# Kernel optimization log

Measured on AMD Instinct MI355X. Metric: run time of the kernel, lower is better.

## Reference

```python
import jax, jax.numpy as jnp
import numpy as np


def setup_inputs() -> dict:
    key = jax.random.key(0)
    ks = jax.random.split(key, 8)
    B, Te, De, Dd, H = 64, 1024, 1024, 1024, 1024
    return {
        "encoder_outputs": jax.random.normal(ks[0], (B, Te, De), jnp.float32),
        "decoder_outputs": jax.random.normal(ks[1], (B, 1, Dd), jnp.float32),
        "Wa_w": jax.random.normal(ks[2], (H, Dd), jnp.float32) * 0.02,
        "Wa_b": jax.random.normal(ks[3], (H,), jnp.float32) * 0.02,
        "Ua_w": jax.random.normal(ks[4], (H, De), jnp.float32) * 0.02,
        "Ua_b": jax.random.normal(ks[5], (H,), jnp.float32) * 0.02,
        "Va_w": jax.random.normal(ks[6], (1, H), jnp.float32) * 0.02,
        "Va_b": jax.random.normal(ks[7], (1,), jnp.float32) * 0.02,
    }


def reference(encoder_outputs, decoder_outputs, Wa_w, Wa_b, Ua_w, Ua_b, Va_w, Va_b):
    # Wa: [B,1,H], Ua: [B,Te,H]  (torch Linear: x @ W.T + b)
    Wa = jnp.einsum('bqd,hd->bqh', decoder_outputs, Wa_w) + Wa_b
    Ua = jnp.einsum('bed,hd->beh', encoder_outputs, Ua_w) + Ua_b
    # broadcast add -> tanh -> scalar score per encoder position: [B,Te,1]
    scores = jnp.einsum('beh,oh->beo', jnp.tanh(Wa + Ua), Va_w) + Va_b
    scores = jnp.transpose(scores, (0, 2, 1))          # [B,1,Te]
    weights = jax.nn.softmax(scores, axis=-1)          # softmax over Te
    context = jnp.einsum('bqe,bed->bqd', weights, encoder_outputs)  # [B,1,De]
    return context
```

## Files before the change

### kernel.cpp

```cpp
#include <hip/hip_runtime.h>
#include <hip/hip_bf16.h>

#define B_  64
#define TE  1024
#define K_  1024
#define HH  1024
#define MM  (B_ * TE)

typedef __bf16 bf16x8 __attribute__((ext_vector_type(8)));
typedef __bf16 bf16x4 __attribute__((ext_vector_type(4)));
typedef float  f32x4  __attribute__((ext_vector_type(4)));

__device__ __forceinline__ float fast_tanh(float x) {
    float ax = __builtin_fabsf(x);
    float t  = __expf(-2.0f * ax);
    float r  = (1.0f - t) * __builtin_amdgcn_rcpf(1.0f + t);
    return __builtin_copysignf(r, x);
}

#define SWZ(r) ((((r) & 3)) ^ ((((r) >> 2)) & 3))

__global__ void cvt_kernel(const float* __restrict__ in, __bf16* __restrict__ out, long n4) {
    long i = (long)blockIdx.x * blockDim.x + threadIdx.x;
    long stride = (long)gridDim.x * blockDim.x;
    const float4* in4 = (const float4*)in;
    bf16x4* out4 = (bf16x4*)out;
    for (long j = i; j < n4; j += stride) {
        float4 v = in4[j];
        bf16x4 o;
        o[0] = (__bf16)v.x; o[1] = (__bf16)v.y; o[2] = (__bf16)v.z; o[3] = (__bf16)v.w;
        out4[j] = o;
    }
}

__global__ __launch_bounds__(256) void wa_kernel(const float* __restrict__ dec,
                                                 const float* __restrict__ Wa_w,
                                                 const float* __restrict__ Wa_b,
                                                 float* __restrict__ WaOut) {
    int b = blockIdx.x, hc = blockIdx.y;
    int wave = threadIdx.x >> 6, lane = threadIdx.x & 63;

    const float4* d4 = (const float4*)(dec + b * 1024);
    float4 dreg[4];
    #pragma unroll
    for (int j = 0; j < 4; j++) dreg[j] = d4[lane * 4 + j];

    #pragma unroll 4
    for (int i = 0; i < 16; i++) {
        int h = hc * 64 + wave * 16 + i;
        const float4* wr = (const float4*)(Wa_w + (long)h * 1024);
        float a = 0.0f;
        #pragma unroll
        for (int j = 0; j < 4; j++) {
            float4 v = wr[lane * 4 + j];
            a += v.x * dreg[j].x + v.y * dreg[j].y + v.z * dreg[j].z + v.w * dreg[j].w;
        }
        #pragma unroll
        for (int off = 32; off > 0; off >>= 1)
            a += __shfl_xor(a, off, 64);
        if (lane == 0) WaOut[b * 1024 + h] = a + Wa_b[h];
    }
}

#define MT 128
#define NP 256
#define KT 32
#define NSTEP (K_ / KT)

__global__ __launch_bounds__(256, 2) void score_gemm(
    const float* __restrict__ Af,
    __bf16* __restrict__ encB,
    const __bf16* __restrict__ Bm,
    const float* __restrict__ Wa,
    const float* __restrict__ Ua_b,
    const float* __restrict__ Va_w,
    float* __restrict__ scores)
{
    __shared__ __bf16 sA[2][MT * KT];
    __shared__ __bf16 sB[2][NP * KT];
    __shared__ float sVa[NP];
    __shared__ float sWU[NP];

    const int tid  = threadIdx.x;
    const int wave = tid >> 6;
    const int lane = tid & 63;
    const int quad = lane >> 4;
    const int l16  = lane & 15;
    const int wm   = wave >> 1;
    const int wn   = wave & 1;
    const int slotq = quad ^ SWZ(l16);

    const int bid = blockIdx.x;
    const int grp = bid >> 5;
    const int r5  = bid & 31;
    const int y   = r5 >> 3;
    const int x   = grp * 8 + (r5 & 7);

    const int rowBase = x * MT;
    const int colBase = y * NP;
    const int b       = rowBase >> 10;
    const bool wb     = (y == 0);

    if (tid < NP) {
        int h = colBase + tid;
        sVa[tid] = Va_w[h];
        sWU[tid] = Wa[b * 1024 + h] + Ua_b[h];
    }

    const long aBase = (long)rowBase * K_;
    const long bBase = (long)colBase * K_;

    int rrA[2], sgA[2];
    #pragma unroll
    for (int i = 0; i < 2; i++) {
        int c = i * 256 + tid;
        rrA[i] = c >> 2;
        sgA[i] = (c & 3) ^ SWZ(rrA[i]);
    }

    float4 pre[2][2];

    auto loadA = [&](int tk) {
        int k = tk * KT;
        #pragma unroll
        for (int i = 0; i < 2; i++) {
            const float4* p = (const float4*)(Af + aBase + (long)rrA[i] * K_ + k + sgA[i] * 8);
            pre[i][0] = p[0]; pre[i][1] = p[1];
        }
    };
    auto cvtA = [&](__bf16* sAn, int tk) {
        int k = tk * KT;
        #pragma unroll
        for (int i = 0; i < 2; i++) {
            bf16x8 v;
            v[0] = (__bf16)pre[i][0].x; v[1] = (__bf16)pre[i][0].y;
            v[2] = (__bf16)pre[i][0].z; v[3] = (__bf16)pre[i][0].w;
            v[4] = (__bf16)pre[i][1].x; v[5] = (__bf16)pre[i][1].y;
            v[6] = (__bf16)pre[i][1].z; v[7] = (__bf16)pre[i][1].w;
            *(bf16x8*)(sAn + (i * 256 + tid) * 8) = v;
            if (wb)
                *(bf16x8*)(encB + aBase + (long)rrA[i] * K_ + k + sgA[i] * 8) = v;
        }
    };
    auto stageB = [&](__bf16* sBn, int tk) {
        int k = tk * KT;
        #pragma unroll
        for (int i = 0; i < 4; i++) {
            int c = i * 256 + tid;
            int r = c >> 2;
            int seg = (c & 3) ^ SWZ(r);
            __builtin_amdgcn_global_load_lds(
                (const __attribute__((address_space(1))) unsigned int*)(Bm + bBase + (long)r * K_ + k + seg * 8),
                (__attribute__((address_space(3))) unsigned int*)(sBn + c * 8), 16, 0, 0);
        }
    };

    f32x4 acc[4][8] = {};

    loadA(0);
    stageB(sB[0], 0);
    cvtA(sA[0], 0);
    loadA(1);
    __syncthreads();

    #pragma unroll 2
    for (int t = 0; t < NSTEP; ++t) {
        const int cur = t & 1, nxt = cur ^ 1;

        if (t < NSTEP - 1) {
            stageB(sB[nxt], t + 1);
            cvtA(sA[nxt], t + 1);
            if (t < NSTEP - 2) loadA(t + 2);
        }

        bf16x8 bfr[8];
        #pragma unroll
        for (int t8 = 0; t8 < 8; t8++) {
            int r = wn * 128 + t8 * 16 + l16;
            bfr[t8] = *(const bf16x8*)(sB[cur] + r * KT + slotq * 8);
        }
        #pragma unroll
        for (int s = 0; s < 4; s++) {
            int r = wm * 64 + s * 16 + l16;
            bf16x8 af = *(const bf16x8*)(sA[cur] + r * KT + slotq * 8);
            #pragma unroll
            for (int t8 = 0; t8 < 8; t8++)
                acc[s][t8] = __builtin_amdgcn_mfma_f32_16x16x32_bf16(af, bfr[t8], acc[s][t8], 0, 0, 0);
        }
        __syncthreads();
    }

    float rs[4][4] = {};
    #pragma unroll
    for (int s = 0; s < 4; s++)
        #pragma unroll
        for (int t = 0; t < 8; t++) {
            int hl = wn * 128 + t * 16 + l16;
            float va = sVa[hl], wu = sWU[hl];
            #pragma unroll
            for (int r = 0; r < 4; r++)
                rs[s][r] += va * fast_tanh(acc[s][t][r] + wu);
        }

    #pragma unroll
    for (int s = 0; s < 4; s++)
        #pragma unroll
        for (int r = 0; r < 4; r++) {
            float v = rs[s][r];
            v += __shfl_xor(v, 1, 64);
            v += __shfl_xor(v, 2, 64);
            v += __shfl_xor(v, 4, 64);
            v += __shfl_xor(v, 8, 64);
            if (l16 == 0)
                atomicAdd(&scores[rowBase + wm * 64 + s * 16 + quad * 4 + r], v);
        }
}

__global__ void softmax_kernel(float* __restrict__ s) {
    __shared__ float red[256];
    int b = blockIdx.x, tid = threadIdx.x;
    float4* row = (float4*)(s + b * 1024);
    float4 v = row[tid];
    float m = fmaxf(fmaxf(v.x, v.y), fmaxf(v.z, v.w));
    red[tid] = m; __syncthreads();
    for (int off = 128; off > 0; off >>= 1) {
        if (tid < off) red[tid] = fmaxf(red[tid], red[tid + off]);
        __syncthreads();
    }
    m = red[0]; __syncthreads();
    v.x = expf(v.x - m); v.y = expf(v.y - m); v.z = expf(v.z - m); v.w = expf(v.w - m);
    red[tid] = v.x + v.y + v.z + v.w; __syncthreads();
    for (int off = 128; off > 0; off >>= 1) {
        if (tid < off) red[tid] += red[tid + off];
        __syncthreads();
    }
    float inv = 1.0f / red[0];
    v.x *= inv; v.y *= inv; v.z *= inv; v.w *= inv;
    row[tid] = v;
}

__global__ __launch_bounds__(256) void context_partial(const __bf16* __restrict__ enc,
                                                       const float* __restrict__ w,
                                                       float* __restrict__ pb) {
    __shared__ float red[2][128][8];
    int b = blockIdx.x, ec = blockIdx.y, tid = threadIdx.x;
    int eo = tid >> 7;
    int dc = tid & 127;
    const bf16x8* enc8 = (const bf16x8*)(enc + ((long)b * 1024 + ec * 128) * 1024);
    const float* wrow = w + b * 1024 + ec * 128;
    float acc[8] = {};
    #pragma unroll 4
    for (int e = eo; e < 128; e += 2) {
        float we = wrow[e];
        bf16x8 v = enc8[e * 128 + dc];
        #pragma unroll
        for (int j = 0; j < 8; j++) acc[j] += we * (float)v[j];
    }
    #pragma unroll
    for (int j = 0; j < 8; j++) red[eo][dc][j] = acc[j];
    __syncthreads();
    if (eo == 0) {
        float* o = pb + ((long)(b * 8 + ec)) * 1024 + dc * 8;
        #pragma unroll
        for (int j = 0; j < 8; j++) o[j] = red[0][dc][j] + red[1][dc][j];
    }
}

__global__ void context_reduce(const float* __restrict__ pb, float* __restrict__ out) {
    int b = blockIdx.x, tid = threadIdx.x;
    const f32x4* p4 = (const f32x4*)pb;
    f32x4 s = {0.f, 0.f, 0.f, 0.f};
    #pragma unroll
    for (int ec = 0; ec < 8; ec++)
        s += p4[(b * 8 + ec) * 256 + tid];
    ((f32x4*)out)[b * 256 + tid] = s;
}

extern "C" void kernel_launch(void* const* d_in, const int* in_sizes, int n_in,
                              void* d_out, int out_size, void* d_ws, size_t ws_size,
                              hipStream_t stream) {
    (void)in_sizes; (void)n_in; (void)ws_size;
    const float* enc   = (const float*)d_in[0];
    const float* dec   = (const float*)d_in[1];
    const float* Wa_w  = (const float*)d_in[2];
    const float* Wa_b  = (const float*)d_in[3];
    const float* Ua_w  = (const float*)d_in[4];
    const float* Ua_b  = (const float*)d_in[5];
    const float* Va_w  = (const float*)d_in[6];
    float* out = (float*)d_out;

    char* w = (char*)d_ws;
    __bf16* encB = (__bf16*)w;  w += (size_t)MM * 1024 * 2;
    __bf16* uawB = (__bf16*)w;  w += (size_t)HH * 1024 * 2;
    float* WaBuf = (float*)w;   w += (size_t)B_ * HH * 4;
    float* scores = (float*)w;  w += (size_t)MM * 4;
    float* pb = (float*)w;      w += (size_t)B_ * 8 * 1024 * 4;

    hipMemsetAsync(scores, 0, (size_t)MM * 4, stream);
    cvt_kernel<<<dim3(256), 256, 0, stream>>>(Ua_w, uawB, (long)HH * 1024 / 4);
    wa_kernel<<<dim3(B_, 16), 256, 0, stream>>>(dec, Wa_w, Wa_b, WaBuf);
    score_gemm<<<dim3((MM / MT) * (HH / NP)), 256, 0, stream>>>(enc, encB, uawB, WaBuf, Ua_b, Va_w, scores);
    softmax_kernel<<<dim3(B_), 256, 0, stream>>>(scores);
    context_partial<<<dim3(B_, 8), 256, 0, stream>>>(encB, scores, pb);
    context_reduce<<<dim3(B_), 256, 0, stream>>>(pb, out);
}
```

Measured before the change: 611.3 us.

## Restructure score GEMM pipeline, change LDS swizzle, fuse prep kernels, shuffle softmax

```diff
diff --git a/kernel.cpp b/kernel.cpp
--- a/kernel.cpp
+++ b/kernel.cpp
@@ -18,27 +18,28 @@
     return __builtin_copysignf(r, x);
 }
 
-#define SWZ(r) ((((r) & 3)) ^ ((((r) >> 2)) & 3))
-
-__global__ void cvt_kernel(const float* __restrict__ in, __bf16* __restrict__ out, long n4) {
-    long i = (long)blockIdx.x * blockDim.x + threadIdx.x;
-    long stride = (long)gridDim.x * blockDim.x;
-    const float4* in4 = (const float4*)in;
-    bf16x4* out4 = (bf16x4*)out;
-    for (long j = i; j < n4; j += stride) {
-        float4 v = in4[j];
-        bf16x4 o;
-        o[0] = (__bf16)v.x; o[1] = (__bf16)v.y; o[2] = (__bf16)v.z; o[3] = (__bf16)v.w;
-        out4[j] = o;
-    }
-}
-
-__global__ __launch_bounds__(256) void wa_kernel(const float* __restrict__ dec,
-                                                 const float* __restrict__ Wa_w,
-                                                 const float* __restrict__ Wa_b,
-                                                 float* __restrict__ WaOut) {
-    int b = blockIdx.x, hc = blockIdx.y;
-    int wave = threadIdx.x >> 6, lane = threadIdx.x & 63;
+__global__ __launch_bounds__(256) void prep_kernel(const float* __restrict__ Ua_w,
+                                                   __bf16* __restrict__ uawB,
+                                                   const float* __restrict__ dec,
+                                                   const float* __restrict__ Wa_w,
+                                                   const float* __restrict__ Wa_b,
+                                                   float* __restrict__ WaOut) {
+    int bid = blockIdx.x, tid = threadIdx.x;
+    if (bid < 256) {
+        const long n4 = (long)HH * 1024 / 4;
+        const float4* in4 = (const float4*)Ua_w;
+        bf16x4* out4 = (bf16x4*)uawB;
+        for (long j = bid * 256 + tid; j < n4; j += 65536) {
+            float4 v = in4[j];
+            bf16x4 o;
+            o[0] = (__bf16)v.x; o[1] = (__bf16)v.y; o[2] = (__bf16)v.z; o[3] = (__bf16)v.w;
+            out4[j] = o;
+        }
+        return;
+    }
+    int wb = bid - 256;
+    int b = wb >> 4, hc = wb & 15;
+    int wave = tid >> 6, lane = tid & 63;
 
     const float4* d4 = (const float4*)(dec + b * 1024);
     float4 dreg[4];
@@ -66,6 +67,7 @@
 #define NP 256
 #define KT 32
 #define NSTEP (K_ / KT)
+#define SWZ(r) (((r) >> 1) & 3)
 
 __global__ __launch_bounds__(256, 2) void score_gemm(
     const float* __restrict__ Af,
@@ -88,7 +90,6 @@
     const int l16  = lane & 15;
     const int wm   = wave >> 1;
     const int wn   = wave & 1;
-    const int slotq = quad ^ SWZ(l16);
 
     const int bid = blockIdx.x;
     const int grp = bid >> 5;
@@ -107,9 +108,6 @@
         sWU[tid] = Wa[b * 1024 + h] + Ua_b[h];
     }
 
-    const long aBase = (long)rowBase * K_;
-    const long bBase = (long)colBase * K_;
-
     int rrA[2], sgA[2];
     #pragma unroll
     for (int i = 0; i < 2; i++) {
@@ -117,6 +115,9 @@
         rrA[i] = c >> 2;
         sgA[i] = (c & 3) ^ SWZ(rrA[i]);
     }
+
+    const long aBase = (long)rowBase * K_;
+    const long bBase = (long)colBase * K_;
 
     float4 pre[2][2];
 
@@ -157,38 +158,57 @@
 
     f32x4 acc[4][8] = {};
 
+    auto compute = [&](const __bf16* sAc, const __bf16* sBc) {
+        bf16x8 bfr[8];
+        #pragma unroll
+        for (int t8 = 0; t8 < 8; t8++) {
+            int r = wn * 128 + t8 * 16 + l16;
+            int slot = quad ^ SWZ(r);
+            bfr[t8] = *(const bf16x8*)(sBc + r * KT + slot * 8);
+        }
+        #pragma unroll
+        for (int s = 0; s < 4; s++) {
+            int r = wm * 64 + s * 16 + l16;
+            int slot = quad ^ SWZ(r);
+            bf16x8 af = *(const bf16x8*)(sAc + r * KT + slot * 8);
+            #pragma unroll
+            for (int t8 = 0; t8 < 8; t8++)
+                acc[s][t8] = __builtin_amdgcn_mfma_f32_16x16x32_bf16(af, bfr[t8], acc[s][t8], 0, 0, 0);
+        }
+    };
+
     loadA(0);
     stageB(sB[0], 0);
     cvtA(sA[0], 0);
     loadA(1);
-    __syncthreads();
+    stageB(sB[1], 1);
+    asm volatile("s_waitcnt vmcnt(8) lgkmcnt(0)" ::: "memory");
+    __builtin_amdgcn_sched_barrier(0);
+    __builtin_amdgcn_s_barrier();
+    asm volatile("" ::: "memory");
 
     #pragma unroll 2
-    for (int t = 0; t < NSTEP; ++t) {
+    for (int t = 0; t < NSTEP - 2; ++t) {
         const int cur = t & 1, nxt = cur ^ 1;
-
-        if (t < NSTEP - 1) {
-            stageB(sB[nxt], t + 1);
-            cvtA(sA[nxt], t + 1);
-            if (t < NSTEP - 2) loadA(t + 2);
-        }
-
-        bf16x8 bfr[8];
-        #pragma unroll
-        for (int t8 = 0; t8 < 8; t8++) {
-            int r = wn * 128 + t8 * 16 + l16;
-            bfr[t8] = *(const bf16x8*)(sB[cur] + r * KT + slotq * 8);
-        }
-        #pragma unroll
-        for (int s = 0; s < 4; s++) {
-            int r = wm * 64 + s * 16 + l16;
-            bf16x8 af = *(const bf16x8*)(sA[cur] + r * KT + slotq * 8);
-            #pragma unroll
-            for (int t8 = 0; t8 < 8; t8++)
-                acc[s][t8] = __builtin_amdgcn_mfma_f32_16x16x32_bf16(af, bfr[t8], acc[s][t8], 0, 0, 0);
-        }
-        __syncthreads();
-    }
+        compute(sA[cur], sB[cur]);
+        cvtA(sA[nxt], t + 1);
+        loadA(t + 2);
+        asm volatile("s_waitcnt vmcnt(4) lgkmcnt(0)" ::: "memory");
+        __builtin_amdgcn_sched_barrier(0);
+        __builtin_amdgcn_s_barrier();
+        asm volatile("" ::: "memory");
+        stageB(sB[cur], t + 2);
+    }
+    {
+        const int cur = (NSTEP - 2) & 1, nxt = cur ^ 1;
+        compute(sA[cur], sB[cur]);
+        cvtA(sA[nxt], NSTEP - 1);
+        asm volatile("s_waitcnt vmcnt(0) lgkmcnt(0)" ::: "memory");
+        __builtin_amdgcn_sched_barrier(0);
+        __builtin_amdgcn_s_barrier();
+        asm volatile("" ::: "memory");
+    }
+    compute(sA[(NSTEP - 1) & 1], sB[(NSTEP - 1) & 1]);
 
     float rs[4][4] = {};
     #pragma unroll
@@ -216,25 +236,27 @@
         }
 }
 
-__global__ void softmax_kernel(float* __restrict__ s) {
-    __shared__ float red[256];
+__global__ __launch_bounds__(256) void softmax_kernel(float* __restrict__ s) {
+    __shared__ float red[8];
     int b = blockIdx.x, tid = threadIdx.x;
+    int wave = tid >> 6, lane = tid & 63;
     float4* row = (float4*)(s + b * 1024);
     float4 v = row[tid];
     float m = fmaxf(fmaxf(v.x, v.y), fmaxf(v.z, v.w));
-    red[tid] = m; __syncthreads();
-    for (int off = 128; off > 0; off >>= 1) {
-        if (tid < off) red[tid] = fmaxf(red[tid], red[tid + off]);
-        __syncthreads();
-    }
-    m = red[0]; __syncthreads();
+    #pragma unroll
+    for (int off = 32; off > 0; off >>= 1)
+        m = fmaxf(m, __shfl_xor(m, off, 64));
+    if (lane == 0) red[wave] = m;
+    __syncthreads();
+    m = fmaxf(fmaxf(red[0], red[1]), fmaxf(red[2], red[3]));
     v.x = expf(v.x - m); v.y = expf(v.y - m); v.z = expf(v.z - m); v.w = expf(v.w - m);
-    red[tid] = v.x + v.y + v.z + v.w; __syncthreads();
-    for (int off = 128; off > 0; off >>= 1) {
-        if (tid < off) red[tid] += red[tid + off];
-        __syncthreads();
-    }
-    float inv = 1.0f / red[0];
+    float sum = v.x + v.y + v.z + v.w;
+    #pragma unroll
+    for (int off = 32; off > 0; off >>= 1)
+        sum += __shfl_xor(sum, off, 64);
+    if (lane == 0) red[4 + wave] = sum;
+    __syncthreads();
+    float inv = 1.0f / (red[4] + red[5] + red[6] + red[7]);
     v.x *= inv; v.y *= inv; v.z *= inv; v.w *= inv;
     row[tid] = v;
 }
@@ -297,8 +319,7 @@
     float* pb = (float*)w;      w += (size_t)B_ * 8 * 1024 * 4;
 
     hipMemsetAsync(scores, 0, (size_t)MM * 4, stream);
-    cvt_kernel<<<dim3(256), 256, 0, stream>>>(Ua_w, uawB, (long)HH * 1024 / 4);
-    wa_kernel<<<dim3(B_, 16), 256, 0, stream>>>(dec, Wa_w, Wa_b, WaBuf);
+    prep_kernel<<<dim3(256 + B_ * 16), 256, 0, stream>>>(Ua_w, uawB, dec, Wa_w, Wa_b, WaBuf);
     score_gemm<<<dim3((MM / MT) * (HH / NP)), 256, 0, stream>>>(enc, encB, uawB, WaBuf, Ua_b, Va_w, scores);
     softmax_kernel<<<dim3(B_), 256, 0, stream>>>(scores);
     context_partial<<<dim3(B_, 8), 256, 0, stream>>>(encB, scores, pb);
```

Measured after the change: 585.0 us. 1.04x faster.
